# Kernel optimization log

Hardware: AMD Instinct MI355X
Metric: run time of the kernel (lower is better)

The kernel has to match this reference:

```python
import jax, jax.numpy as jnp
import numpy as np

CHUNK = 16
GROUPS = 8
EPS = 1e-5


def setup_inputs() -> dict:
    key = jax.random.key(0)
    ks = jax.random.split(key, 8)
    B, C, H, W = 8, 1, 2048, 2048
    D_in = C * CHUNK * CHUNK  # 256
    D = 16                    # out_channels
    x = jax.random.normal(ks[0], (B, C, H, W), dtype=jnp.float32)
    s_fc = 1.0 / np.sqrt(D_in)
    fc_wr = jax.random.normal(ks[1], (D, D_in), dtype=jnp.float32) * s_fc
    fc_wi = jax.random.normal(ks[2], (D, D_in), dtype=jnp.float32) * s_fc
    fc_br = jax.random.normal(ks[3], (D,), dtype=jnp.float32) * s_fc
    fc_bi = jax.random.normal(ks[4], (D,), dtype=jnp.float32) * s_fc
    conv_w = jax.random.normal(ks[5], (D, D), dtype=jnp.float32) * (1.0 / np.sqrt(D))
    conv_b = jax.random.normal(ks[6], (D,), dtype=jnp.float32) * 0.05
    gamma = jnp.ones((D,), dtype=jnp.float32)
    beta = jnp.zeros((D,), dtype=jnp.float32)
    return {"x": x, "fc_wr": fc_wr, "fc_wi": fc_wi, "fc_br": fc_br,
            "fc_bi": fc_bi, "conv_w": conv_w, "conv_b": conv_b,
            "gamma": gamma, "beta": beta}


def reference(x, fc_wr, fc_wi, fc_br, fc_bi, conv_w, conv_b, gamma, beta):
    B, C, H, W = x.shape
    s = CHUNK
    h, w = H // s, W // s
    D = fc_wr.shape[0]
    # rearrange 'b c (h s1) (w s2) -> (b h w) (s1 s2 c)'
    p = x.reshape(B, C, h, s, w, s)
    p = p.transpose(0, 2, 4, 3, 5, 1).reshape(B * h * w, s * s * C)
    # FFT over the flattened patch dim (ortho norm) -> complex64
    fft = jnp.fft.fft(p, norm="ortho")
    Wc = fc_wr + 1j * fc_wi           # [D, D_in] complex
    bc = fc_br + 1j * fc_bi           # [D]
    fc = fft @ Wc.T + bc              # [N, D] complex linear
    # IFFT over channel dim (size D), keep real part
    y = jnp.fft.ifft(fc, norm="ortho").real  # [N, D] float32
    # '(b h w) d -> b d h w'
    y = y.reshape(B, h, w, D).transpose(0, 3, 1, 2)
    # 1x1 conv
    y = jnp.einsum("bdhw,ed->behw", y, conv_w) + conv_b[None, :, None, None]
    # GroupNorm(GROUPS, D)
    yg = y.reshape(B, GROUPS, D // GROUPS, h, w)
    mean = yg.mean(axis=(2, 3, 4), keepdims=True)
    var = yg.var(axis=(2, 3, 4), keepdims=True)
    yn = ((yg - mean) * jax.lax.rsqrt(var + EPS)).reshape(B, D, h, w)
    return yn * gamma[None, :, None, None] + beta[None, :, None, None]
```

## Files before the change

### kernel.cpp

```cpp
#include <hip/hip_runtime.h>
#include <math.h>

#define PI_F 3.14159265358979323846f


#define WS_AH    0
#define WS_U     2048
#define WS_STATS 2112

using half8   = __attribute__((ext_vector_type(8))) _Float16;
using floatx4 = __attribute__((ext_vector_type(4))) float;

__global__ __launch_bounds__(256) void prep(
        const float* __restrict__ wr, const float* __restrict__ wi,
        const float* __restrict__ br, const float* __restrict__ bi,
        const float* __restrict__ cw, const float* __restrict__ cb,
        float* __restrict__ ws) {
    const int e = blockIdx.x;
    const int t = threadIdx.x;
    __shared__ float c16[16], s16[16], Fr[16], Fi[16];
    __shared__ float Gr[256], Gi[256], cosT[256], sinT[256];

    float ang = (2.0f * PI_F / 256.0f) * (float)t;
    cosT[t] = cosf(ang);
    sinT[t] = sinf(ang);
    if (t < 16) {
        float a = (2.0f * PI_F / 16.0f) * (float)t;
        c16[t] = cosf(a);
        s16[t] = sinf(a);
    }
    __syncthreads();

    if (t < 16) {
        float fr = 0.f, fi = 0.f;
        #pragma unroll
        for (int m = 0; m < 16; ++m) {
            float c = cw[e * 16 + m];
            fr += c * c16[(t * m) & 15];
            fi += c * s16[(t * m) & 15];
        }
        Fr[t] = fr;
        Fi[t] = fi;
    }
    __syncthreads();

    {
        float gr = 0.f, gi = 0.f;
        #pragma unroll
        for (int d = 0; d < 16; ++d) {
            float wrv = wr[d * 256 + t];
            float wiv = wi[d * 256 + t];
            gr += wrv * Fr[d] - wiv * Fi[d];
            gi += wrv * Fi[d] + wiv * Fr[d];
        }
        Gr[t] = gr;
        Gi[t] = gi;
    }
    if (t == 0) {
        float s = 0.f;
        #pragma unroll
        for (int d = 0; d < 16; ++d) s += br[d] * Fr[d] - bi[d] * Fi[d];
        ws[WS_U + e] = cb[e] + 0.25f * s;
    }
    __syncthreads();

    float acc = 0.f;
    for (int k = 0; k < 256; ++k) {
        int a = (k * t) & 255;
        acc += Gr[k] * cosT[a] + Gi[k] * sinT[a];
    }
    _Float16* Ah = (_Float16*)(ws + WS_AH);
    Ah[e * 256 + t] = (_Float16)(acc * (1.0f / 64.0f));

    if (e == 0 && t < 128) ws[WS_STATS + t] = 0.f;
}

__global__ __launch_bounds__(256) void main_k(const float* __restrict__ x,
                                              const float* __restrict__ ws,
                                              float* __restrict__ out,
                                              float* __restrict__ stats) {
    __shared__ _Float16 A_sh[16 * 264];
    __shared__ float s_sum[8], s_ssq[8];
    const int t = threadIdx.x;

    {
        const uint4* asrc = (const uint4*)(ws + WS_AH);
        uint4 q0 = asrc[t * 2];
        uint4 q1 = asrc[t * 2 + 1];
        _Float16* dp = A_sh + (t >> 4) * 264 + (t & 15) * 16;
        *(uint4*)dp       = q0;
        *(uint4*)(dp + 8) = q1;
    }
    if (t < 8) { s_sum[t] = 0.f; s_ssq[t] = 0.f; }

    const int w    = t >> 6;
    const int lane = t & 63;
    const int m    = lane & 15;
    const int kg   = lane >> 4;

    const float u = ws[WS_U + m];

    const int P0  = blockIdx.x << 6;
    const int b   = P0 >> 14;
    const int pi  = P0 & 16383;
    const int ph  = pi >> 7;
    const int pw0 = pi & 127;

    const float* xb = x + ((size_t)b << 22)
                        + (size_t)(ph << 4) * 2048
                        + (size_t)((pw0 + w * 16 + m) << 4);
    __syncthreads();

    floatx4 acc = {0.f, 0.f, 0.f, 0.f};
    const int r_off = (kg >> 1);
    const int c_off = (kg & 1) << 3;

    #pragma unroll
    for (int s = 0; s < 8; ++s) {
        const float* px = xb + (size_t)(2 * s + r_off) * 2048 + c_off;
        float4 x0 = *(const float4*)px;
        float4 x1 = *(const float4*)(px + 4);
        half8 a;
        a[0] = (_Float16)x0.x; a[1] = (_Float16)x0.y;
        a[2] = (_Float16)x0.z; a[3] = (_Float16)x0.w;
        a[4] = (_Float16)x1.x; a[5] = (_Float16)x1.y;
        a[6] = (_Float16)x1.z; a[7] = (_Float16)x1.w;
        half8 bf = *(const half8*)&A_sh[m * 264 + s * 32 + kg * 8];
        acc = __builtin_amdgcn_mfma_f32_16x16x32_f16(a, bf, acc, 0, 0, 0);
    }

    float v0 = acc[0] + u;
    float v1 = acc[1] + u;
    float v2 = acc[2] + u;
    float v3 = acc[3] + u;
    *(float4*)&out[((size_t)b << 18) + (size_t)m * 16384
                   + (size_t)(ph << 7) + (size_t)(pw0 + w * 16 + kg * 4)]
        = make_float4(v0, v1, v2, v3);

    float sv = v0 + v1 + v2 + v3;
    float qv = v0 * v0 + v1 * v1 + v2 * v2 + v3 * v3;
    sv += __shfl_xor(sv, 16, 64);  qv += __shfl_xor(qv, 16, 64);
    sv += __shfl_xor(sv, 32, 64);  qv += __shfl_xor(qv, 32, 64);
    sv += __shfl_xor(sv, 1, 64);   qv += __shfl_xor(qv, 1, 64);
    if (kg == 0 && (m & 1) == 0) {
        atomicAdd(&s_sum[m >> 1], sv);
        atomicAdd(&s_ssq[m >> 1], qv);
    }
    __syncthreads();
    if (t < 8) {
        atomicAdd(&stats[b * 8 + t],      s_sum[t]);
        atomicAdd(&stats[64 + b * 8 + t], s_ssq[t]);
    }
}

__global__ __launch_bounds__(256) void finalize(float* __restrict__ out,
                                                const float* __restrict__ stats,
                                                const float* __restrict__ gamma,
                                                const float* __restrict__ beta) {
    const int i    = blockIdx.x * 256 + threadIdx.x;
    const int flat = i << 2;
    const int b = flat >> 18;
    const int c = (flat >> 14) & 15;
    const int g = c >> 1;

    const float inv_n = 1.0f / 32768.0f;
    float mean = stats[b * 8 + g] * inv_n;
    float var  = stats[64 + b * 8 + g] * inv_n - mean * mean;
    float rstd = rsqrtf(var + 1e-5f);
    float sc = rstd * gamma[c];
    float sh = beta[c] - mean * sc;

    float4 vv = ((float4*)out)[i];
    vv.x = vv.x * sc + sh;
    vv.y = vv.y * sc + sh;
    vv.z = vv.z * sc + sh;
    vv.w = vv.w * sc + sh;
    ((float4*)out)[i] = vv;
}

extern "C" void kernel_launch(void* const* d_in, const int* in_sizes, int n_in,
                              void* d_out, int out_size, void* d_ws, size_t ws_size,
                              hipStream_t stream) {
    const float* x  = (const float*)d_in[0];
    const float* wr = (const float*)d_in[1];
    const float* wi = (const float*)d_in[2];
    const float* br = (const float*)d_in[3];
    const float* bi = (const float*)d_in[4];
    const float* cw = (const float*)d_in[5];
    const float* cb = (const float*)d_in[6];
    const float* gm = (const float*)d_in[7];
    const float* bt = (const float*)d_in[8];
    float* out = (float*)d_out;
    float* ws  = (float*)d_ws;

    prep<<<16, 256, 0, stream>>>(wr, wi, br, bi, cw, cb, ws);
    main_k<<<2048, 256, 0, stream>>>(x, ws, out, ws + WS_STATS);
    finalize<<<2048, 256, 0, stream>>>(out, ws + WS_STATS, gm, bt);
}
```

Measured before the change: 223.4 us.

## Fuse GroupNorm finalize into main kernel via per-batch completion barrier

Removes the separate finalize kernel. Each main_k block now keeps its conv outputs in registers, adds its partial sums to the stats, and bumps a per-batch counter. The last block of a batch computes the scale and shift and publishes them through a release flag, while the other blocks spin until it is set and then write normalized output once. This drops one kernel launch and a full read-modify-write pass over the output. In exchange, blocks stall in the spin-wait, and it relies on all 256 blocks of a batch being co-resident, with a deadlock risk if they are not.

Result: slower. 630.5 us (+182.3%).

```diff
diff --git a/kernel.cpp b/kernel.cpp
--- a/kernel.cpp
+++ b/kernel.cpp
@@ -7,6 +7,9 @@
 #define WS_AH    0
 #define WS_U     2048
 #define WS_STATS 2112
+#define WS_CTR   2240
+#define WS_FLAG  2272
+#define WS_PAR   2304
 
 using half8   = __attribute__((ext_vector_type(8))) _Float16;
 using floatx4 = __attribute__((ext_vector_type(4))) float;
@@ -72,13 +75,13 @@
     _Float16* Ah = (_Float16*)(ws + WS_AH);
     Ah[e * 256 + t] = (_Float16)(acc * (1.0f / 64.0f));
 
-    if (e == 0 && t < 128) ws[WS_STATS + t] = 0.f;
+    if (e == 0 && t < 192) ws[WS_STATS + t] = 0.f;
 }
 
-__global__ __launch_bounds__(256) void main_k(const float* __restrict__ x,
-                                              const float* __restrict__ ws,
-                                              float* __restrict__ out,
-                                              float* __restrict__ stats) {
+__global__ __launch_bounds__(256, 2) void main_k(
+        const float* __restrict__ x, float* __restrict__ ws,
+        float* __restrict__ out,
+        const float* __restrict__ gamma, const float* __restrict__ beta) {
     __shared__ _Float16 A_sh[16 * 264];
     __shared__ float s_sum[8], s_ssq[8];
     const int t = threadIdx.x;
@@ -133,9 +136,6 @@
     float v1 = acc[1] + u;
     float v2 = acc[2] + u;
     float v3 = acc[3] + u;
-    *(float4*)&out[((size_t)b << 18) + (size_t)m * 16384
-                   + (size_t)(ph << 7) + (size_t)(pw0 + w * 16 + kg * 4)]
-        = make_float4(v0, v1, v2, v3);
 
     float sv = v0 + v1 + v2 + v3;
     float qv = v0 * v0 + v1 * v1 + v2 * v2 + v3 * v3;
@@ -148,34 +148,55 @@
     }
     __syncthreads();
     if (t < 8) {
-        atomicAdd(&stats[b * 8 + t],      s_sum[t]);
-        atomicAdd(&stats[64 + b * 8 + t], s_ssq[t]);
-    }
-}
-
-__global__ __launch_bounds__(256) void finalize(float* __restrict__ out,
-                                                const float* __restrict__ stats,
-                                                const float* __restrict__ gamma,
-                                                const float* __restrict__ beta) {
-    const int i    = blockIdx.x * 256 + threadIdx.x;
-    const int flat = i << 2;
-    const int b = flat >> 18;
-    const int c = (flat >> 14) & 15;
-    const int g = c >> 1;
-
-    const float inv_n = 1.0f / 32768.0f;
-    float mean = stats[b * 8 + g] * inv_n;
-    float var  = stats[64 + b * 8 + g] * inv_n - mean * mean;
-    float rstd = rsqrtf(var + 1e-5f);
-    float sc = rstd * gamma[c];
-    float sh = beta[c] - mean * sc;
-
-    float4 vv = ((float4*)out)[i];
-    vv.x = vv.x * sc + sh;
-    vv.y = vv.y * sc + sh;
-    vv.z = vv.z * sc + sh;
-    vv.w = vv.w * sc + sh;
-    ((float4*)out)[i] = vv;
+        atomicAdd(&ws[WS_STATS + b * 8 + t],      s_sum[t]);
+        atomicAdd(&ws[WS_STATS + 64 + b * 8 + t], s_ssq[t]);
+    }
+    __threadfence();
+    __syncthreads();
+
+    unsigned* ctr  = (unsigned*)(ws + WS_CTR);
+    unsigned* flag = (unsigned*)(ws + WS_FLAG);
+    float*    par  = ws + WS_PAR + b * 32;
+
+    if (t == 0) {
+        unsigned old = atomicAdd(&ctr[b], 1u);
+        if (old == 255u) {
+            const float inv_n = 1.0f / 32768.0f;
+            #pragma unroll
+            for (int g = 0; g < 8; ++g) {
+                float S = __hip_atomic_load(&ws[WS_STATS + b * 8 + g],
+                                            __ATOMIC_RELAXED, __HIP_MEMORY_SCOPE_AGENT);
+                float Q = __hip_atomic_load(&ws[WS_STATS + 64 + b * 8 + g],
+                                            __ATOMIC_RELAXED, __HIP_MEMORY_SCOPE_AGENT);
+                float mean = S * inv_n;
+                float var  = Q * inv_n - mean * mean;
+                float rstd = rsqrtf(var + 1e-5f);
+                #pragma unroll
+                for (int cc = 0; cc < 2; ++cc) {
+                    int c = 2 * g + cc;
+                    float sc = rstd * gamma[c];
+                    float sh = beta[c] - mean * sc;
+                    __hip_atomic_store(&par[c], sc,
+                                       __ATOMIC_RELAXED, __HIP_MEMORY_SCOPE_AGENT);
+                    __hip_atomic_store(&par[16 + c], sh,
+                                       __ATOMIC_RELAXED, __HIP_MEMORY_SCOPE_AGENT);
+                }
+            }
+            __hip_atomic_store(&flag[b], 1u,
+                               __ATOMIC_RELEASE, __HIP_MEMORY_SCOPE_AGENT);
+        }
+        while (__hip_atomic_load(&flag[b], __ATOMIC_ACQUIRE,
+                                 __HIP_MEMORY_SCOPE_AGENT) == 0u)
+            __builtin_amdgcn_s_sleep(2);
+    }
+    __syncthreads();
+
+    float sc = __hip_atomic_load(&par[m], __ATOMIC_RELAXED, __HIP_MEMORY_SCOPE_AGENT);
+    float sh = __hip_atomic_load(&par[16 + m], __ATOMIC_RELAXED, __HIP_MEMORY_SCOPE_AGENT);
+
+    *(float4*)&out[((size_t)b << 18) + (size_t)m * 16384
+                   + (size_t)(ph << 7) + (size_t)(pw0 + w * 16 + kg * 4)]
+        = make_float4(v0 * sc + sh, v1 * sc + sh, v2 * sc + sh, v3 * sc + sh);
 }
 
 extern "C" void kernel_launch(void* const* d_in, const int* in_sizes, int n_in,
@@ -194,6 +215,5 @@
     float* ws  = (float*)d_ws;
 
     prep<<<16, 256, 0, stream>>>(wr, wi, br, bi, cw, cb, ws);
-    main_k<<<2048, 256, 0, stream>>>(x, ws, out, ws + WS_STATS);
-    finalize<<<2048, 256, 0, stream>>>(out, ws + WS_STATS, gm, bt);
+    main_k<<<2048, 256, 0, stream>>>(x, ws, out, gm, bt);
 }
```

## Stream x tiles into LDS via async global_load_lds with staged vmcnt waits

Applied to the files above, without the earlier changes.

Each wave now issues all sixteen 16-byte loads of its x tile directly into LDS using global_load_lds, then waits on decreasing vmcnt counts so each MFMA step can start as soon as its slice arrives. The A operand is loaded straight from global into registers instead of being staged through shared memory, which drops the block-wide barrier before compute. Shared-memory atomics for per-group statistics are replaced by plain per-wave slot writes that are summed after the barrier. The kernel now needs 64 KB of LDS per block, which may lower occupancy, and it relies on the compiler not issuing other vector-memory loads between the async loads and the hand-written vmcnt waits.

Result: no change. 220.2 us (-1.4%).

```diff
diff --git a/kernel.cpp b/kernel.cpp
--- a/kernel.cpp
+++ b/kernel.cpp
@@ -10,6 +10,13 @@
 
 using half8   = __attribute__((ext_vector_type(8))) _Float16;
 using floatx4 = __attribute__((ext_vector_type(4))) float;
+
+__device__ __forceinline__ void gload_lds16(const void* g, void* l) {
+    __builtin_amdgcn_global_load_lds(
+        (const __attribute__((address_space(1))) uint32_t*)g,
+        (__attribute__((address_space(3))) uint32_t*)l,
+        16, 0, 0);
+}
 
 __global__ __launch_bounds__(256) void prep(
         const float* __restrict__ wr, const float* __restrict__ wi,
@@ -79,25 +86,22 @@
                                               const float* __restrict__ ws,
                                               float* __restrict__ out,
                                               float* __restrict__ stats) {
-    __shared__ _Float16 A_sh[16 * 264];
-    __shared__ float s_sum[8], s_ssq[8];
+    __shared__ float x_sh[4 * 4096];
+    __shared__ float s_sum[4][8], s_ssq[4][8];
     const int t = threadIdx.x;
-
-    {
-        const uint4* asrc = (const uint4*)(ws + WS_AH);
-        uint4 q0 = asrc[t * 2];
-        uint4 q1 = asrc[t * 2 + 1];
-        _Float16* dp = A_sh + (t >> 4) * 264 + (t & 15) * 16;
-        *(uint4*)dp       = q0;
-        *(uint4*)(dp + 8) = q1;
-    }
-    if (t < 8) { s_sum[t] = 0.f; s_ssq[t] = 0.f; }
 
     const int w    = t >> 6;
     const int lane = t & 63;
     const int m    = lane & 15;
     const int kg   = lane >> 4;
-
+    const int r_off = (kg >> 1);
+    const int c_off = (kg & 1) << 3;
+
+    const _Float16* Ah = (const _Float16*)(ws + WS_AH);
+    half8 Areg[8];
+    #pragma unroll
+    for (int s = 0; s < 8; ++s)
+        Areg[s] = *(const half8*)(Ah + m * 256 + s * 32 + kg * 8);
     const float u = ws[WS_U + m];
 
     const int P0  = blockIdx.x << 6;
@@ -109,25 +113,42 @@
     const float* xb = x + ((size_t)b << 22)
                         + (size_t)(ph << 4) * 2048
                         + (size_t)((pw0 + w * 16 + m) << 4);
-    __syncthreads();
+
+    float* lp = x_sh + w * 4096;
+    #pragma unroll
+    for (int j = 0; j < 16; ++j) {
+        const int s = j >> 1, h = j & 1;
+        const float* src = xb + (size_t)(2 * s + r_off) * 2048 + c_off + 4 * h;
+        gload_lds16(src, lp + j * 256);
+    }
 
     floatx4 acc = {0.f, 0.f, 0.f, 0.f};
-    const int r_off = (kg >> 1);
-    const int c_off = (kg & 1) << 3;
-
-    #pragma unroll
-    for (int s = 0; s < 8; ++s) {
-        const float* px = xb + (size_t)(2 * s + r_off) * 2048 + c_off;
-        float4 x0 = *(const float4*)px;
-        float4 x1 = *(const float4*)(px + 4);
-        half8 a;
-        a[0] = (_Float16)x0.x; a[1] = (_Float16)x0.y;
-        a[2] = (_Float16)x0.z; a[3] = (_Float16)x0.w;
-        a[4] = (_Float16)x1.x; a[5] = (_Float16)x1.y;
-        a[6] = (_Float16)x1.z; a[7] = (_Float16)x1.w;
-        half8 bf = *(const half8*)&A_sh[m * 264 + s * 32 + kg * 8];
-        acc = __builtin_amdgcn_mfma_f32_16x16x32_f16(a, bf, acc, 0, 0, 0);
-    }
+    const float* xw = x_sh + w * 4096 + lane * 4;
+
+#define WAITVM(N) asm volatile("s_waitcnt vmcnt(" #N ")" ::: "memory")
+#define STEP(S, VM) do {                                                 \
+        WAITVM(VM);                                                      \
+        const float4 c0 = *(const float4*)(xw + (S) * 512);              \
+        const float4 c1 = *(const float4*)(xw + (S) * 512 + 256);        \
+        half8 a;                                                         \
+        a[0] = (_Float16)c0.x; a[1] = (_Float16)c0.y;                    \
+        a[2] = (_Float16)c0.z; a[3] = (_Float16)c0.w;                    \
+        a[4] = (_Float16)c1.x; a[5] = (_Float16)c1.y;                    \
+        a[6] = (_Float16)c1.z; a[7] = (_Float16)c1.w;                    \
+        acc = __builtin_amdgcn_mfma_f32_16x16x32_f16(a, Areg[S], acc,    \
+                                                     0, 0, 0);           \
+    } while (0)
+
+    STEP(0, 14);
+    STEP(1, 12);
+    STEP(2, 10);
+    STEP(3, 8);
+    STEP(4, 6);
+    STEP(5, 4);
+    STEP(6, 2);
+    STEP(7, 0);
+#undef STEP
+#undef WAITVM
 
     float v0 = acc[0] + u;
     float v1 = acc[1] + u;
@@ -143,13 +164,15 @@
     sv += __shfl_xor(sv, 32, 64);  qv += __shfl_xor(qv, 32, 64);
     sv += __shfl_xor(sv, 1, 64);   qv += __shfl_xor(qv, 1, 64);
     if (kg == 0 && (m & 1) == 0) {
-        atomicAdd(&s_sum[m >> 1], sv);
-        atomicAdd(&s_ssq[m >> 1], qv);
+        s_sum[w][m >> 1] = sv;
+        s_ssq[w][m >> 1] = qv;
     }
     __syncthreads();
     if (t < 8) {
-        atomicAdd(&stats[b * 8 + t],      s_sum[t]);
-        atomicAdd(&stats[64 + b * 8 + t], s_ssq[t]);
+        float S = s_sum[0][t] + s_sum[1][t] + s_sum[2][t] + s_sum[3][t];
+        float Q = s_ssq[0][t] + s_ssq[1][t] + s_ssq[2][t] + s_ssq[3][t];
+        atomicAdd(&stats[b * 8 + t],      S);
+        atomicAdd(&stats[64 + b * 8 + t], Q);
     }
 }
 
```
